# Performance work log

Hardware: AMD Instinct MI355X
Metric: run time of the kernel (lower is better)

## Reference

```python
import jax, jax.numpy as jnp
import numpy as np

GAM1 = 1.0
GAM2 = 1.0
EPS = 0.01


def setup_inputs() -> dict:
    key = jax.random.key(0)
    k1, k2 = jax.random.split(key)
    m, p, k = 262144, 128, 10
    x = jax.random.normal(k1, (m, p), dtype=jnp.float32)
    y = jax.random.randint(k2, (m,), 0, k, dtype=jnp.int32)
    return {"x": x, "y": y, "num_classes": k}


def reference(x, y, num_classes):
    m, p = x.shape
    I = jnp.eye(p, dtype=x.dtype)
    scalar = p / (m * EPS)

    # W = x.T, so W @ W.T == x.T @ x  (p x p Gram)
    cov = x.T @ x
    discrimn_empi = jnp.linalg.slogdet(I + GAM1 * scalar * cov)[1] / 2.0
    discrimn_theo = jnp.linalg.slogdet(I + scalar * cov)[1] / 2.0

    # per-class compress loss: logdet(I + p/(n_j*eps) * W_j W_j^T) * n_j / m
    onehot = jax.nn.one_hot(y, num_classes, dtype=x.dtype)  # [m, k]
    counts = onehot.sum(axis=0)                             # [k]

    def class_cov(col):  # col: [m] 0/1 mask for one class
        return (x * col[:, None]).T @ x  # [p, p]

    covs = jax.lax.map(class_cov, onehot.T)  # [k, p, p], sequential over k classes

    safe_counts = jnp.maximum(counts, 1.0)
    scal = p / (safe_counts * EPS)                              # [k]
    lds = jnp.linalg.slogdet(I[None] + scal[:, None, None] * covs)[1]  # [k]
    compress = jnp.sum(jnp.where(counts > 0, lds * counts / m, 0.0)) / 2.0

    total_loss_empi = GAM2 * (-discrimn_empi) + compress
    return total_loss_empi, discrimn_empi, discrimn_theo, compress
```

## Files before the change

### kernel.cpp

```cpp
#include <hip/hip_runtime.h>

#define K 10
#define P 128
#define EPSV 0.01f
#define GAM1 1.0f
#define GAM2 1.0f
#define CH 512
#define SK 64
#define KS 68
#define SORTCH 2048
#define NTHR 256

typedef __attribute__((ext_vector_type(8))) short bf16x8;
typedef __attribute__((ext_vector_type(4))) short s16x4;
typedef __attribute__((ext_vector_type(4))) float f32x4;

static __device__ __forceinline__ short f2bf(float f) {
    unsigned u = __float_as_uint(f);
    u = (u + 0x7FFFu + ((u >> 16) & 1u)) >> 16;
    return (short)u;
}

static __device__ __forceinline__ float rdlane(float v, int srclane) {
    return __int_as_float(__builtin_amdgcn_readlane(__float_as_int(v), srclane));
}

__global__ void hist_kernel(const int* __restrict__ y, int* __restrict__ blk_counts, int m) {
    __shared__ int h[K];
    int t = threadIdx.x;
    if (t < K) h[t] = 0;
    __syncthreads();
    int base = blockIdx.x * SORTCH;
    int rows = min(SORTCH, m - base);
    for (int i = t; i < rows; i += NTHR) atomicAdd(&h[y[base + i]], 1);
    __syncthreads();
    if (t < K) blk_counts[blockIdx.x * K + t] = h[t];
}

__global__ void scan_kernel(const int* __restrict__ blk_counts, int* __restrict__ blk_offsets,
                            int* __restrict__ counts, int* __restrict__ pstart, int nb) {
    __shared__ int s[K][128];
    __shared__ int sps[K + 1];
    int t = threadIdx.x;
    int own[K];
    if (t < 128) {
        for (int c = 0; c < K; ++c) {
            int v = (t < nb) ? blk_counts[t * K + c] : 0;
            own[c] = v;
            s[c][t] = v;
        }
    }
    __syncthreads();
    for (int off = 1; off < 128; off <<= 1) {
        int tmp[K];
        if (t < 128)
            for (int c = 0; c < K; ++c) tmp[c] = (t >= off) ? s[c][t - off] : 0;
        __syncthreads();
        if (t < 128)
            for (int c = 0; c < K; ++c) s[c][t] += tmp[c];
        __syncthreads();
    }
    if (t == 0) {
        int run = 0;
        for (int c = 0; c < K; ++c) {
            sps[c] = run;
            int tot = s[c][127];
            counts[c] = tot;
            pstart[c] = run;
            run += ((tot + CH - 1) / CH) * CH;
        }
        sps[K] = run;
        pstart[K] = run;
    }
    __syncthreads();
    if (t < nb)
        for (int c = 0; c < K; ++c)
            blk_offsets[t * K + c] = sps[c] + s[c][t] - own[c];
}

__global__ void scatter_kernel(const int* __restrict__ y, const int* __restrict__ blk_offsets,
                               int* __restrict__ perm, int m) {
    __shared__ int cur[K];
    int t = threadIdx.x;
    if (t < K) cur[t] = blk_offsets[blockIdx.x * K + t];
    __syncthreads();
    int base = blockIdx.x * SORTCH;
    int rows = min(SORTCH, m - base);
    for (int i = t; i < rows; i += NTHR) {
        int row = base + i;
        int pos = atomicAdd(&cur[y[row]], 1);
        perm[pos] = row;
    }
}

__global__ __launch_bounds__(NTHR) void gram_kernel(const float* __restrict__ x,
                                                    const int* __restrict__ perm,
                                                    const int* __restrict__ pstart,
                                                    float* __restrict__ grams) {
    __shared__ int pm[CH];
    __shared__ short xsT[P * KS];
    int t = threadIdx.x;
    long base = (long)blockIdx.x * CH;
    int cls = 0;
    for (int c = 1; c < K; ++c)
        if (base >= (long)pstart[c]) cls = c;
    for (int i = t; i < CH; i += NTHR) pm[i] = perm[base + i];

    const int lane = t & 63;
    const int wave = t >> 6;
    const int m16 = lane & 15;
    const int quad = lane >> 4;
    const int wr = wave >> 1;
    const int wc = wave & 1;
    const int c2 = t & 63;
    const int rg = t >> 6;

    f32x4 acc[4][4];
#pragma unroll
    for (int a = 0; a < 4; ++a)
#pragma unroll
        for (int b = 0; b < 4; ++b) acc[a][b] = (f32x4){0.f, 0.f, 0.f, 0.f};

    __syncthreads();

    for (int s = 0; s < CH / SK; ++s) {
        int sb = s * SK;
        float2 v[16];
#pragma unroll
        for (int ii = 0; ii < 16; ++ii) {
            int r = pm[sb + rg * 16 + ii];
            if (r >= 0) v[ii] = ((const float2*)(x + (size_t)r * P))[c2];
            else { v[ii].x = 0.f; v[ii].y = 0.f; }
        }
        __syncthreads();
        short b0[16], b1[16];
#pragma unroll
        for (int ii = 0; ii < 16; ++ii) { b0[ii] = f2bf(v[ii].x); b1[ii] = f2bf(v[ii].y); }
        int col0 = 2 * c2, col1 = 2 * c2 + 1;
#pragma unroll
        for (int q = 0; q < 4; ++q) {
            s16x4 w0 = {b0[q * 4], b0[q * 4 + 1], b0[q * 4 + 2], b0[q * 4 + 3]};
            s16x4 w1 = {b1[q * 4], b1[q * 4 + 1], b1[q * 4 + 2], b1[q * 4 + 3]};
            *(s16x4*)&xsT[col0 * KS + rg * 16 + q * 4] = w0;
            *(s16x4*)&xsT[col1 * KS + rg * 16 + q * 4] = w1;
        }
        __syncthreads();
#pragma unroll
        for (int kk = 0; kk < 2; ++kk) {
            int k0 = kk * 32 + quad * 8;
            bf16x8 af[4], bfr[4];
#pragma unroll
            for (int a = 0; a < 4; ++a) {
                int colA = wr * 64 + a * 16 + m16;
                union { bf16x8 v8; s16x4 h[2]; } u;
                u.h[0] = *(s16x4*)&xsT[colA * KS + k0];
                u.h[1] = *(s16x4*)&xsT[colA * KS + k0 + 4];
                af[a] = u.v8;
            }
#pragma unroll
            for (int b = 0; b < 4; ++b) {
                int colB = wc * 64 + b * 16 + m16;
                union { bf16x8 v8; s16x4 h[2]; } u;
                u.h[0] = *(s16x4*)&xsT[colB * KS + k0];
                u.h[1] = *(s16x4*)&xsT[colB * KS + k0 + 4];
                bfr[b] = u.v8;
            }
#pragma unroll
            for (int a = 0; a < 4; ++a)
#pragma unroll
                for (int b = 0; b < 4; ++b)
                    acc[a][b] = __builtin_amdgcn_mfma_f32_16x16x32_bf16(af[a], bfr[b], acc[a][b], 0, 0, 0);
        }
    }
    float* g = grams + (size_t)cls * P * P;
#pragma unroll
    for (int a = 0; a < 4; ++a)
#pragma unroll
        for (int b = 0; b < 4; ++b)
#pragma unroll
            for (int r = 0; r < 4; ++r) {
                int gi = wr * 64 + a * 16 + quad * 4 + r;
                int gj = wc * 64 + b * 16 + m16;
                if (gi <= gj) atomicAdd(&g[gi * P + gj], acc[a][b][r]);
            }
}

__global__ void sum_kernel(const float* __restrict__ grams, float* __restrict__ gsum) {
    int idx = blockIdx.x * 256 + threadIdx.x;
    float s = 0.f;
#pragma unroll
    for (int c = 0; c < K; ++c) s += grams[c * P * P + idx];
    gsum[idx] = s;
}

__global__ __launch_bounds__(256, 1) void logdet_kernel(const float* __restrict__ grams,
                                                        const float* __restrict__ gsum,
                                                        const int* __restrict__ counts,
                                                        float* __restrict__ logd, int m) {
    __shared__ float A[P * P];
    int t = threadIdx.x, b = blockIdx.x;
    float scale;
    if (b == 0) scale = GAM1 * (float)P / ((float)m * EPSV);
    else if (b == 1) scale = (float)P / ((float)m * EPSV);
    else {
        float cnt = (float)counts[b - 2];
        if (cnt < 1.f) cnt = 1.f;
        scale = (float)P / (cnt * EPSV);
    }
    const float* src = (b < 2) ? gsum : (grams + (size_t)(b - 2) * P * P);
    for (int idx = t; idx < P * P; idx += 256) {
        int i = idx >> 7, c = idx & (P - 1);
        int s2 = (i <= c) ? idx : (c * P + i);
        A[idx] = scale * src[s2] + ((i == c) ? 1.f : 0.f);
    }
    __syncthreads();

    const int lane = t & 63;
    const int wid = t >> 6;
    float lsum = 0.f;

    for (int bs = 0; bs < 4; ++bs) {
        const int j0 = bs * 32;
        if (wid == 0) {
            float a[32];
            if (lane < 32) {
#pragma unroll
                for (int cc = 0; cc < 8; ++cc)
                    *(f32x4*)&a[cc * 4] = *(f32x4*)&A[(j0 + lane) * P + j0 + cc * 4];
            } else {
#pragma unroll
                for (int cc = 0; cc < 32; ++cc) a[cc] = 0.f;
            }
            float myinv = 0.f;
#pragma unroll
            for (int tt = 0; tt < 32; ++tt) {
                float utt = rdlane(a[tt], tt);
                float inv = __builtin_amdgcn_rcpf(utt);
                lsum += __logf(utt);
                if (lane == tt) myinv = inv;
                bool act = (lane < 32) && (lane > tt);
                float lm = act ? a[tt] * inv : 0.f;
                if (act) a[tt] = lm;
#pragma unroll
                for (int k2 = tt + 1; k2 < 32; ++k2) {
                    float utk = rdlane(a[k2], tt);
                    a[k2] -= lm * utk;
                }
            }
            if (lane < 32) A[(j0 + lane) * P + j0 + lane] = myinv;

            if (bs < 3) {
                int nc = P - j0 - 32;
                int c0 = j0 + 32 + lane;
                int c1 = c0 + 64;
                bool v0 = lane < nc;
                bool v1 = lane + 64 < nc;
                int c0a = v0 ? c0 : (j0 + 32);
                int c1a = v1 ? c1 : (j0 + 32);
                float ua[32], ub[32];
#pragma unroll
                for (int j = 0; j < 32; ++j) {
                    ua[j] = A[(j0 + j) * P + c0a];
                    ub[j] = A[(j0 + j) * P + c1a];
                }
#pragma unroll
                for (int j = 0; j < 32; ++j) {
#pragma unroll
                    for (int t2 = 0; t2 < j; ++t2) {
                        float ljt = rdlane(a[t2], j);
                        ua[j] -= ljt * ua[t2];
                        ub[j] -= ljt * ub[t2];
                    }
                }
#pragma unroll
                for (int j = 0; j < 32; ++j) {
                    if (v0) A[(j0 + j) * P + c0] = ua[j];
                    if (v1) A[(j0 + j) * P + c1] = ub[j];
                }
            }
        }
        __syncthreads();

        if (bs < 3) {
            int nc = P - j0 - 32;
            int nt = nc >> 2;
            int ntiles = nt * nt;
            for (int tile = t; tile < ntiles; tile += 256) {
                int ti = tile / nt, tk = tile - ti * nt;
                int i0 = j0 + 32 + ti * 4, k0 = j0 + 32 + tk * 4;
                f32x4 acc0 = {0, 0, 0, 0}, acc1 = {0, 0, 0, 0};
                f32x4 acc2 = {0, 0, 0, 0}, acc3 = {0, 0, 0, 0};
#pragma unroll
                for (int j = 0; j < 32; ++j) {
                    const float* row = &A[(j0 + j) * P];
                    float invd = row[j0 + j];
                    f32x4 ui = *(const f32x4*)&row[i0];
                    f32x4 uk = *(const f32x4*)&row[k0];
                    uk *= invd;
                    acc0 += ui[0] * uk;
                    acc1 += ui[1] * uk;
                    acc2 += ui[2] * uk;
                    acc3 += ui[3] * uk;
                }
                f32x4* r0 = (f32x4*)&A[(i0 + 0) * P + k0];
                f32x4* r1 = (f32x4*)&A[(i0 + 1) * P + k0];
                f32x4* r2 = (f32x4*)&A[(i0 + 2) * P + k0];
                f32x4* r3 = (f32x4*)&A[(i0 + 3) * P + k0];
                *r0 -= acc0; *r1 -= acc1; *r2 -= acc2; *r3 -= acc3;
            }
            __syncthreads();
        }
    }
    if (t == 0) logd[b] = lsum;
}

__global__ void final_kernel(const float* __restrict__ logd, const int* __restrict__ counts,
                             float* __restrict__ out, int m) {
    if (threadIdx.x == 0 && blockIdx.x == 0) {
        float empi = 0.5f * logd[0];
        float theo = 0.5f * logd[1];
        float comp = 0.f;
        for (int c = 0; c < K; ++c) {
            float cnt = (float)counts[c];
            if (cnt > 0.f) comp += logd[2 + c] * cnt / (float)m;
        }
        comp *= 0.5f;
        out[0] = GAM2 * (-empi) + comp;
        out[1] = empi;
        out[2] = theo;
        out[3] = comp;
    }
}

extern "C" void kernel_launch(void* const* d_in, const int* in_sizes, int n_in,
                              void* d_out, int out_size, void* d_ws, size_t ws_size,
                              hipStream_t stream) {
    const float* x = (const float*)d_in[0];
    const int* y = (const int*)d_in[1];
    int m = in_sizes[1];
    int nbs = (m + SORTCH - 1) / SORTCH;
    int nbg = (m + CH - 1) / CH + K;

    char* ws = (char*)d_ws;
    float* grams = (float*)ws;
    float* gsum = (float*)(ws + 655360);
    float* logd = (float*)(ws + 720896);
    int* counts = (int*)(ws + 720960);
    int* pstart = (int*)(ws + 721024);
    int* blk_counts = (int*)(ws + 721152);
    int* blk_offsets = (int*)(ws + 721152 + (size_t)nbs * K * 4);
    int* perm = (int*)(ws + 721152 + 2 * (size_t)nbs * K * 4);

    hipMemsetAsync(ws, 0, 655360, stream);
    hipMemsetAsync(perm, 0xFF, (size_t)nbg * CH * 4, stream);

    hist_kernel<<<nbs, NTHR, 0, stream>>>(y, blk_counts, m);
    scan_kernel<<<1, NTHR, 0, stream>>>(blk_counts, blk_offsets, counts, pstart, nbs);
    scatter_kernel<<<nbs, NTHR, 0, stream>>>(y, blk_offsets, perm, m);
    gram_kernel<<<nbg, NTHR, 0, stream>>>(x, perm, pstart, grams);
    sum_kernel<<<P * P / 256, 256, 0, stream>>>(grams, gsum);
    logdet_kernel<<<K + 2, 256, 0, stream>>>(grams, gsum, counts, logd, m);
    final_kernel<<<1, 1, 0, stream>>>(logd, counts, (float*)d_out, m);
}
```

Before: 299.4 us.

## Double-buffer gram kernel LDS tiles with register prefetch and smaller chunks

Restructures the gram kernel into a software pipeline. The next stage's rows are loaded from global memory into registers while MFMAs consume the current LDS buffer, and LDS is double-buffered so only one barrier per stage is needed. The chunk and stage sizes are halved, which launches more blocks and raises the occupancy hint to 4. Padding rows are now detected by comparing against per-class count limits, which removes the perm memset, at the cost of twice as many atomic flushes of partial grams to global memory.

Result: slower. 314.2 us (+4.9%).

```diff
diff --git a/kernel.cpp b/kernel.cpp
--- a/kernel.cpp
+++ b/kernel.cpp
@@ -5,9 +5,10 @@
 #define EPSV 0.01f
 #define GAM1 1.0f
 #define GAM2 1.0f
-#define CH 512
-#define SK 64
-#define KS 68
+#define CH 256
+#define SK 32
+#define KS 36
+#define NSTG (CH / SK)
 #define SORTCH 2048
 #define NTHR 256
 
@@ -93,18 +94,21 @@
     }
 }
 
-__global__ __launch_bounds__(NTHR) void gram_kernel(const float* __restrict__ x,
-                                                    const int* __restrict__ perm,
-                                                    const int* __restrict__ pstart,
-                                                    float* __restrict__ grams) {
+__global__ __launch_bounds__(NTHR, 4) void gram_kernel(const float* __restrict__ x,
+                                                       const int* __restrict__ perm,
+                                                       const int* __restrict__ pstart,
+                                                       const int* __restrict__ counts,
+                                                       float* __restrict__ grams) {
     __shared__ int pm[CH];
-    __shared__ short xsT[P * KS];
+    __shared__ short xsT[2][P * KS];
     int t = threadIdx.x;
-    long base = (long)blockIdx.x * CH;
+    int base = blockIdx.x * CH;
     int cls = 0;
+#pragma unroll
     for (int c = 1; c < K; ++c)
-        if (base >= (long)pstart[c]) cls = c;
-    for (int i = t; i < CH; i += NTHR) pm[i] = perm[base + i];
+        if (base >= pstart[c]) cls = c;
+    const int limit = pstart[cls] + counts[cls];
+    pm[t] = perm[base + t];
 
     const int lane = t & 63;
     const int wave = t >> 6;
@@ -112,8 +116,7 @@
     const int quad = lane >> 4;
     const int wr = wave >> 1;
     const int wc = wave & 1;
-    const int c2 = t & 63;
-    const int rg = t >> 6;
+    const int c2 = lane;
 
     f32x4 acc[4][4];
 #pragma unroll
@@ -123,53 +126,69 @@
 
     __syncthreads();
 
-    for (int s = 0; s < CH / SK; ++s) {
-        int sb = s * SK;
-        float2 v[16];
-#pragma unroll
-        for (int ii = 0; ii < 16; ++ii) {
-            int r = pm[sb + rg * 16 + ii];
-            if (r >= 0) v[ii] = ((const float2*)(x + (size_t)r * P))[c2];
-            else { v[ii].x = 0.f; v[ii].y = 0.f; }
+    float2 v[8];
+#pragma unroll
+    for (int ii = 0; ii < 8; ++ii) {
+        int pos = wave * 8 + ii;
+        float2 val; val.x = 0.f; val.y = 0.f;
+        if (base + pos < limit) {
+            int r = pm[pos];
+            val = ((const float2*)(x + (size_t)r * P))[c2];
+        }
+        v[ii] = val;
+    }
+
+#pragma unroll 2
+    for (int s = 0; s < NSTG; ++s) {
+        short* xb = &xsT[s & 1][0];
+        short b0[8], b1[8];
+#pragma unroll
+        for (int ii = 0; ii < 8; ++ii) { b0[ii] = f2bf(v[ii].x); b1[ii] = f2bf(v[ii].y); }
+        {
+            int col0 = 2 * c2, col1 = 2 * c2 + 1;
+            int kb = wave * 8;
+#pragma unroll
+            for (int q = 0; q < 2; ++q) {
+                s16x4 w0 = {b0[q * 4], b0[q * 4 + 1], b0[q * 4 + 2], b0[q * 4 + 3]};
+                s16x4 w1 = {b1[q * 4], b1[q * 4 + 1], b1[q * 4 + 2], b1[q * 4 + 3]};
+                *(s16x4*)&xb[col0 * KS + kb + q * 4] = w0;
+                *(s16x4*)&xb[col1 * KS + kb + q * 4] = w1;
+            }
         }
         __syncthreads();
-        short b0[16], b1[16];
-#pragma unroll
-        for (int ii = 0; ii < 16; ++ii) { b0[ii] = f2bf(v[ii].x); b1[ii] = f2bf(v[ii].y); }
-        int col0 = 2 * c2, col1 = 2 * c2 + 1;
-#pragma unroll
-        for (int q = 0; q < 4; ++q) {
-            s16x4 w0 = {b0[q * 4], b0[q * 4 + 1], b0[q * 4 + 2], b0[q * 4 + 3]};
-            s16x4 w1 = {b1[q * 4], b1[q * 4 + 1], b1[q * 4 + 2], b1[q * 4 + 3]};
-            *(s16x4*)&xsT[col0 * KS + rg * 16 + q * 4] = w0;
-            *(s16x4*)&xsT[col1 * KS + rg * 16 + q * 4] = w1;
-        }
-        __syncthreads();
-#pragma unroll
-        for (int kk = 0; kk < 2; ++kk) {
-            int k0 = kk * 32 + quad * 8;
-            bf16x8 af[4], bfr[4];
-#pragma unroll
-            for (int a = 0; a < 4; ++a) {
-                int colA = wr * 64 + a * 16 + m16;
-                union { bf16x8 v8; s16x4 h[2]; } u;
-                u.h[0] = *(s16x4*)&xsT[colA * KS + k0];
-                u.h[1] = *(s16x4*)&xsT[colA * KS + k0 + 4];
-                af[a] = u.v8;
-            }
-#pragma unroll
-            for (int b = 0; b < 4; ++b) {
-                int colB = wc * 64 + b * 16 + m16;
-                union { bf16x8 v8; s16x4 h[2]; } u;
-                u.h[0] = *(s16x4*)&xsT[colB * KS + k0];
-                u.h[1] = *(s16x4*)&xsT[colB * KS + k0 + 4];
-                bfr[b] = u.v8;
-            }
-#pragma unroll
-            for (int a = 0; a < 4; ++a)
-#pragma unroll
-                for (int b = 0; b < 4; ++b)
-                    acc[a][b] = __builtin_amdgcn_mfma_f32_16x16x32_bf16(af[a], bfr[b], acc[a][b], 0, 0, 0);
+        if (s + 1 < NSTG) {
+            int sb = (s + 1) * SK;
+#pragma unroll
+            for (int ii = 0; ii < 8; ++ii) {
+                int pos = sb + wave * 8 + ii;
+                float2 val; val.x = 0.f; val.y = 0.f;
+                if (base + pos < limit) {
+                    int r = pm[pos];
+                    val = ((const float2*)(x + (size_t)r * P))[c2];
+                }
+                v[ii] = val;
+            }
+        }
+        int k0 = quad * 8;
+        bf16x8 bfr[4];
+#pragma unroll
+        for (int b = 0; b < 4; ++b) {
+            int colB = wc * 64 + b * 16 + m16;
+            union { bf16x8 v8; s16x4 h[2]; } u;
+            u.h[0] = *(const s16x4*)&xb[colB * KS + k0];
+            u.h[1] = *(const s16x4*)&xb[colB * KS + k0 + 4];
+            bfr[b] = u.v8;
+        }
+#pragma unroll
+        for (int a = 0; a < 4; ++a) {
+            int colA = wr * 64 + a * 16 + m16;
+            union { bf16x8 v8; s16x4 h[2]; } u;
+            u.h[0] = *(const s16x4*)&xb[colA * KS + k0];
+            u.h[1] = *(const s16x4*)&xb[colA * KS + k0 + 4];
+            bf16x8 af = u.v8;
+#pragma unroll
+            for (int b = 0; b < 4; ++b)
+                acc[a][b] = __builtin_amdgcn_mfma_f32_16x16x32_bf16(af, bfr[b], acc[a][b], 0, 0, 0);
         }
     }
     float* g = grams + (size_t)cls * P * P;
@@ -352,12 +371,11 @@
     int* perm = (int*)(ws + 721152 + 2 * (size_t)nbs * K * 4);
 
     hipMemsetAsync(ws, 0, 655360, stream);
-    hipMemsetAsync(perm, 0xFF, (size_t)nbg * CH * 4, stream);
 
     hist_kernel<<<nbs, NTHR, 0, stream>>>(y, blk_counts, m);
     scan_kernel<<<1, NTHR, 0, stream>>>(blk_counts, blk_offsets, counts, pstart, nbs);
     scatter_kernel<<<nbs, NTHR, 0, stream>>>(y, blk_offsets, perm, m);
-    gram_kernel<<<nbg, NTHR, 0, stream>>>(x, perm, pstart, grams);
+    gram_kernel<<<nbg, NTHR, 0, stream>>>(x, perm, pstart, counts, grams);
     sum_kernel<<<P * P / 256, 256, 0, stream>>>(grams, gsum);
     logdet_kernel<<<K + 2, 256, 0, stream>>>(grams, gsum, counts, logd, m);
     final_kernel<<<1, 1, 0, stream>>>(logd, counts, (float*)d_out, m);
```
